# Optimization experiments

Measured on AMD Instinct MI355X. Metric: run time of the kernel, lower is better.

The kernel has to match this reference:

```python
import jax, jax.numpy as jnp
import numpy as np

VOCAB = 50257
D_MEAN = 1024
D_MV = 1024
BATCH = 32
SEQ_LEN = 128


def setup_inputs() -> dict:
    key = jax.random.key(0)
    k_z, k_lab, k_w0, k_w1 = jax.random.split(key, 4)
    z = jax.random.normal(k_z, (BATCH, D_MEAN), dtype=jnp.float32)
    labels = jax.random.randint(k_lab, (BATCH, SEQ_LEN), 0, VOCAB, dtype=jnp.int64)
    # Linear weights stored as [in, out]; scaled like kaiming-uniform-ish init
    W0 = jax.random.normal(k_w0, (D_MEAN, D_MV), dtype=jnp.float32) * (1.0 / np.sqrt(D_MEAN))
    b0 = jnp.zeros((D_MV,), dtype=jnp.float32)
    W1 = jax.random.normal(k_w1, (D_MV, VOCAB), dtype=jnp.float32) * (1.0 / np.sqrt(D_MV))
    b1 = jnp.zeros((VOCAB,), dtype=jnp.float32)
    return {"z": z, "labels": labels, "W0": W0, "b0": b0, "W1": W1, "b1": b1}


def reference(z, labels, W0, b0, W1, b1):
    # bow_head: Linear -> Dropout(eval=identity) -> GELU -> Linear -> Dropout
    h = jax.nn.gelu(z @ W0 + b0, approximate=False)        # [B, d_mean_var]
    logits = h @ W1 + b1                                   # [B, vocab]
    # CrossEntropyLoss over logits expanded across seq_len == mean over
    # (B*seq_len) of NLL; log_softmax computed once per batch row and the
    # label gather reused across seq_len (same math, no expand materialized).
    logp = jax.nn.log_softmax(logits, axis=-1)             # [B, vocab]
    nll = -jnp.take_along_axis(logp, labels, axis=1)       # [B, seq_len]
    return jnp.mean(nll)
```

## Files before the change

kernel.cpp:

```cpp
#include <hip/hip_runtime.h>
#include <math.h>

#define VOCAB 50257
#define DMEAN 1024
#define DMV   1024
#define BATCH 32
#define SEQLEN 128
#define NS1 32
#define NS2 8
#define KC2 (DMV / NS2)
#define CH3 2048
#define VP  51200
#define VPH (VP / 2)
#define NB3 (VP / CH3)

static __device__ inline unsigned f2bf(float x) {
    unsigned u = __float_as_uint(x);
    return (u + 0x7fffu + ((u >> 16) & 1u)) >> 16;
}

__global__ __launch_bounds__(256) void k1_partial(const float* __restrict__ z,
                                                  const float* __restrict__ W0,
                                                  float* __restrict__ part) {
    int tx = threadIdx.x;
    int j  = blockIdx.x * 256 + tx;
    int k0 = blockIdx.y * (DMEAN / NS1);
    float acc[BATCH];
#pragma unroll
    for (int r = 0; r < BATCH; ++r) acc[r] = 0.f;
#pragma unroll 8
    for (int k = k0; k < k0 + (DMEAN / NS1); ++k) {
        float w = W0[k * DMV + j];
#pragma unroll
        for (int r = 0; r < BATCH; ++r)
            acc[r] = fmaf(z[r * DMEAN + k], w, acc[r]);
    }
#pragma unroll
    for (int r = 0; r < BATCH; ++r)
        part[(blockIdx.y * BATCH + r) * DMV + j] = acc[r];
}

__global__ __launch_bounds__(256) void k1_combine(const float* __restrict__ part,
                                                  const float* __restrict__ b0,
                                                  float* __restrict__ hT) {
    int t  = blockIdx.x * 256 + threadIdx.x;
    int e0 = t * 4;
    int r  = e0 >> 10;
    int j  = e0 & 1023;
    float4 s = *(const float4*)(b0 + j);
#pragma unroll
    for (int kb = 0; kb < NS1; ++kb) {
        float4 p = *(const float4*)(part + kb * BATCH * DMV + e0);
        s.x += p.x; s.y += p.y; s.z += p.z; s.w += p.w;
    }
    float v[4] = {s.x, s.y, s.z, s.w};
#pragma unroll
    for (int u = 0; u < 4; ++u) {
        float g = 0.5f * v[u] * (1.f + erff(v[u] * 0.70710678118654752f));
        hT[(j + u) * BATCH + r] = g;
    }
}

__global__ __launch_bounds__(256, 6) void k2_part(const float* __restrict__ hT,
                                                  const float* __restrict__ W1,
                                                  unsigned* __restrict__ part2) {
    __shared__ float hs[KC2 * BATCH];
    int tx = threadIdx.x;
    int n  = blockIdx.x * 256 + tx;
    int nn = min(n, VOCAB - 1);
    int k0 = blockIdx.y * KC2;

    {
        const float4* src = (const float4*)(hT + (size_t)k0 * BATCH);
        float4*       dst = (float4*)hs;
#pragma unroll
        for (int i = 0; i < (KC2 * BATCH / 4) / 256; ++i)
            dst[tx + i * 256] = src[tx + i * 256];
    }
    __syncthreads();

    float acc[BATCH];
#pragma unroll
    for (int r = 0; r < BATCH; ++r) acc[r] = 0.f;

    const float* w = W1 + (size_t)k0 * VOCAB + nn;
#pragma unroll 8
    for (int k = 0; k < KC2; ++k) {
        float wv = w[(size_t)k * VOCAB];
        const float4* hk = (const float4*)(hs + k * BATCH);
        float4 h4[8];
#pragma unroll
        for (int q = 0; q < 8; ++q) h4[q] = hk[q];
        const float* hv = (const float*)h4;
#pragma unroll
        for (int r = 0; r < BATCH; ++r)
            acc[r] = fmaf(hv[r], wv, acc[r]);
    }

    unsigned* p = part2 + (size_t)blockIdx.y * BATCH * VPH + (n >> 1);
    bool even = (tx & 1) == 0;
#pragma unroll
    for (int r = 0; r < BATCH; ++r) {
        float other = __shfl_xor(acc[r], 1, 64);
        unsigned pk = f2bf(acc[r]) | (f2bf(other) << 16);
        if (even) p[(size_t)r * VPH] = pk;
    }
}

__device__ inline float block_reduce_sum(float v, float* red) {
    int tx = threadIdx.x;
#pragma unroll
    for (int off = 32; off > 0; off >>= 1) v += __shfl_down(v, off, 64);
    if ((tx & 63) == 0) red[tx >> 6] = v;
    __syncthreads();
    float res = (red[0] + red[1]) + (red[2] + red[3]);
    __syncthreads();
    return res;
}

__global__ __launch_bounds__(256) void k3_stream(const unsigned* __restrict__ part2,
                                                 const float* __restrict__ b1,
                                                 const int* __restrict__ labels,
                                                 float* __restrict__ se_out,
                                                 float* __restrict__ g_out) {
    __shared__ float sval[CH3];
    __shared__ float red[4];
    int chunk = blockIdx.x, r = blockIdx.y, tx = threadIdx.x;
    int n0 = chunk * CH3 + tx * 8;

    float v[8];
#pragma unroll
    for (int u = 0; u < 8; ++u) v[u] = 0.f;
#pragma unroll
    for (int cs = 0; cs < NS2; ++cs) {
        const unsigned* base = part2 + ((size_t)cs * BATCH + r) * VPH + (n0 >> 1);
        uint4 pv = *(const uint4*)base;
        unsigned pw[4] = {pv.x, pv.y, pv.z, pv.w};
#pragma unroll
        for (int q = 0; q < 4; ++q) {
            v[2 * q]     += __uint_as_float(pw[q] << 16);
            v[2 * q + 1] += __uint_as_float(pw[q] & 0xffff0000u);
        }
    }

    float e = 0.f;
    if (n0 + 7 < VOCAB) {
        float4 ba = *(const float4*)(b1 + n0);
        float4 bb = *(const float4*)(b1 + n0 + 4);
        float bv[8] = {ba.x, ba.y, ba.z, ba.w, bb.x, bb.y, bb.z, bb.w};
#pragma unroll
        for (int u = 0; u < 8; ++u) {
            float lg = v[u] + bv[u];
            sval[tx * 8 + u] = lg;
            e += expf(lg);
        }
    } else {
#pragma unroll
        for (int u = 0; u < 8; ++u) {
            int n = n0 + u;
            float lg = (n < VOCAB) ? (v[u] + b1[n]) : 0.f;
            sval[tx * 8 + u] = lg;
            if (n < VOCAB) e += expf(lg);
        }
    }
    e = block_reduce_sum(e, red);
    if (tx == 0) se_out[r * NB3 + chunk] = e;

    float g = 0.f;
    if (tx < SEQLEN) {
        int lab = labels[r * SEQLEN + tx];
        unsigned d = (unsigned)(lab - chunk * CH3);
        if (d < (unsigned)CH3) g = sval[d];
    }
    g = block_reduce_sum(g, red);
    if (tx == 0) g_out[chunk * BATCH + r] = g;
}

__global__ __launch_bounds__(256) void k4_final(const float* __restrict__ se,
                                                const float* __restrict__ g_part,
                                                float* __restrict__ out) {
    __shared__ float red[4];
    __shared__ float lses[BATCH];
    int tx = threadIdx.x;
    int r = tx >> 3, l8 = tx & 7;
    float s = 0.f;
    for (int c = l8; c < NB3; c += 8) s += se[r * NB3 + c];
#pragma unroll
    for (int off = 4; off > 0; off >>= 1) s += __shfl_down(s, off, 8);
    if (l8 == 0) lses[r] = logf(s);

    float g = 0.f;
    for (int i = tx; i < NB3 * BATCH; i += 256) g += g_part[i];
    g = block_reduce_sum(g, red);

    if (tx == 0) {
        float L = 0.f;
#pragma unroll
        for (int r2 = 0; r2 < BATCH; ++r2) L += lses[r2];
        out[0] = ((float)SEQLEN * L - g) / (float)(BATCH * SEQLEN);
    }
}

extern "C" void kernel_launch(void* const* d_in, const int* in_sizes, int n_in,
                              void* d_out, int out_size, void* d_ws, size_t ws_size,
                              hipStream_t stream) {
    const float* z      = (const float*)d_in[0];
    const int*   labels = (const int*)  d_in[1];
    const float* W0     = (const float*)d_in[2];
    const float* b0     = (const float*)d_in[3];
    const float* W1     = (const float*)d_in[4];
    const float* b1     = (const float*)d_in[5];
    float* out = (float*)d_out;
    float* ws  = (float*)d_ws;

    float*    part1 = ws;
    float*    hT    = part1 + (size_t)NS1 * BATCH * DMV;
    unsigned* part2 = (unsigned*)(hT + (size_t)DMV * BATCH);
    float*    se    = (float*)(part2 + (size_t)NS2 * BATCH * VPH);
    float*    gpart = se + (size_t)BATCH * NB3;

    k1_partial<<<dim3(4, NS1), 256, 0, stream>>>(z, W0, part1);
    k1_combine<<<32, 256, 0, stream>>>(part1, b0, hT);
    k2_part<<<dim3((VOCAB + 255) / 256, NS2), 256, 0, stream>>>(hT, W1, part2);
    k3_stream<<<dim3(NB3, BATCH), 256, 0, stream>>>(part2, b1, labels, se, gpart);
    k4_final<<<1, 256, 0, stream>>>(se, gpart, out);
}
```

Measured before the change: 101.2 us.

## Replace FP32 FMA vocab GEMM with bf16 MFMA using bf16 hidden activations

The second linear layer now runs on the matrix cores via 16x16x32 bf16 MFMA instructions. The hidden activations are stored row-major in bf16, and W1 is loaded as fp32 and converted to bf16 in registers. This targets the scalar-FMA compute bottleneck in the 32x1024x50257 product. It reduces the precision of both operands to bf16, and the strided W1 loads per lane may be less coalesced.

```diff
diff --git a/kernel.cpp b/kernel.cpp
--- a/kernel.cpp
+++ b/kernel.cpp
@@ -14,6 +14,9 @@
 #define VPH (VP / 2)
 #define NB3 (VP / CH3)
 
+typedef __attribute__((ext_vector_type(8))) short short8v;
+typedef __attribute__((ext_vector_type(4))) float f32x4;
+
 static __device__ inline unsigned f2bf(float x) {
     unsigned u = __float_as_uint(x);
     return (u + 0x7fffu + ((u >> 16) & 1u)) >> 16;
@@ -42,7 +45,7 @@
 
 __global__ __launch_bounds__(256) void k1_combine(const float* __restrict__ part,
                                                   const float* __restrict__ b0,
-                                                  float* __restrict__ hT) {
+                                                  unsigned short* __restrict__ hB) {
     int t  = blockIdx.x * 256 + threadIdx.x;
     int e0 = t * 4;
     int r  = e0 >> 10;
@@ -54,56 +57,82 @@
         s.x += p.x; s.y += p.y; s.z += p.z; s.w += p.w;
     }
     float v[4] = {s.x, s.y, s.z, s.w};
+    unsigned b[4];
 #pragma unroll
     for (int u = 0; u < 4; ++u) {
         float g = 0.5f * v[u] * (1.f + erff(v[u] * 0.70710678118654752f));
-        hT[(j + u) * BATCH + r] = g;
-    }
-}
-
-__global__ __launch_bounds__(256, 6) void k2_part(const float* __restrict__ hT,
+        b[u] = f2bf(g);
+    }
+    *(uint2*)(hB + (size_t)r * DMV + j) =
+        make_uint2(b[0] | (b[1] << 16), b[2] | (b[3] << 16));
+}
+
+__global__ __launch_bounds__(256, 4) void k2_mfma(const unsigned short* __restrict__ hB,
                                                   const float* __restrict__ W1,
                                                   unsigned* __restrict__ part2) {
-    __shared__ float hs[KC2 * BATCH];
-    int tx = threadIdx.x;
-    int n  = blockIdx.x * 256 + tx;
-    int nn = min(n, VOCAB - 1);
-    int k0 = blockIdx.y * KC2;
-
-    {
-        const float4* src = (const float4*)(hT + (size_t)k0 * BATCH);
-        float4*       dst = (float4*)hs;
-#pragma unroll
-        for (int i = 0; i < (KC2 * BATCH / 4) / 256; ++i)
-            dst[tx + i * 256] = src[tx + i * 256];
-    }
-    __syncthreads();
-
-    float acc[BATCH];
-#pragma unroll
-    for (int r = 0; r < BATCH; ++r) acc[r] = 0.f;
-
-    const float* w = W1 + (size_t)k0 * VOCAB + nn;
-#pragma unroll 8
-    for (int k = 0; k < KC2; ++k) {
-        float wv = w[(size_t)k * VOCAB];
-        const float4* hk = (const float4*)(hs + k * BATCH);
-        float4 h4[8];
-#pragma unroll
-        for (int q = 0; q < 8; ++q) h4[q] = hk[q];
-        const float* hv = (const float*)h4;
-#pragma unroll
-        for (int r = 0; r < BATCH; ++r)
-            acc[r] = fmaf(hv[r], wv, acc[r]);
-    }
-
-    unsigned* p = part2 + (size_t)blockIdx.y * BATCH * VPH + (n >> 1);
-    bool even = (tx & 1) == 0;
-#pragma unroll
-    for (int r = 0; r < BATCH; ++r) {
-        float other = __shfl_xor(acc[r], 1, 64);
-        unsigned pk = f2bf(acc[r]) | (f2bf(other) << 16);
-        if (even) p[(size_t)r * VPH] = pk;
+    int tx   = threadIdx.x;
+    int lane = tx & 63;
+    int w    = tx >> 6;
+    int lr   = lane & 15;
+    int lg   = lane >> 4;
+    int k0   = blockIdx.y * KC2;
+    int col0 = blockIdx.x * 256 + w * 64;
+
+    short8v a[2][4];
+#pragma unroll
+    for (int m = 0; m < 2; ++m)
+#pragma unroll
+        for (int t = 0; t < 4; ++t) {
+            const unsigned* hp =
+                (const unsigned*)(hB + (size_t)(m * 16 + lr) * DMV + k0 + t * 32 + lg * 4);
+            union { short8v v; unsigned u[4]; } A;
+            A.u[0] = hp[0];  A.u[1] = hp[1];
+            A.u[2] = hp[8];  A.u[3] = hp[9];
+            a[m][t] = A.v;
+        }
+
+    f32x4 acc[4][2];
+#pragma unroll
+    for (int c = 0; c < 4; ++c)
+#pragma unroll
+        for (int m = 0; m < 2; ++m)
+            acc[c][m] = (f32x4){0.f, 0.f, 0.f, 0.f};
+
+#pragma unroll
+    for (int c = 0; c < 4; ++c) {
+        unsigned colc = (unsigned)min(col0 + c * 16 + lr, VOCAB - 1);
+        const float* wl = W1 + (size_t)(k0 + lg * 4) * VOCAB + colc;
+#pragma unroll
+        for (int t = 0; t < 4; ++t) {
+            float fv[8];
+#pragma unroll
+            for (int r = 0; r < 8; ++r)
+                fv[r] = wl[(size_t)(t * 32 + (r & 3) + 16 * (r >> 2)) * VOCAB];
+            union { short8v v; unsigned u[4]; } B;
+#pragma unroll
+            for (int q = 0; q < 4; ++q)
+                B.u[q] = f2bf(fv[2 * q]) | (f2bf(fv[2 * q + 1]) << 16);
+            acc[c][0] = __builtin_amdgcn_mfma_f32_16x16x32_bf16(a[0][t], B.v, acc[c][0], 0, 0, 0);
+            acc[c][1] = __builtin_amdgcn_mfma_f32_16x16x32_bf16(a[1][t], B.v, acc[c][1], 0, 0, 0);
+        }
+    }
+
+    unsigned* pb = part2 + (size_t)blockIdx.y * BATCH * VPH;
+#pragma unroll
+    for (int c = 0; c < 4; ++c) {
+        int col = col0 + c * 16 + lr;
+#pragma unroll
+        for (int m = 0; m < 2; ++m) {
+            int row0 = m * 16 + lg * 4;
+#pragma unroll
+            for (int j = 0; j < 4; ++j) {
+                float v = acc[c][m][j];
+                float o = __shfl_xor(v, 1, 64);
+                if (!(lane & 1))
+                    pb[(size_t)(row0 + j) * VPH + (col >> 1)] =
+                        f2bf(v) | (f2bf(o) << 16);
+            }
+        }
     }
 }
 
@@ -213,15 +242,15 @@
     float* out = (float*)d_out;
     float* ws  = (float*)d_ws;
 
-    float*    part1 = ws;
-    float*    hT    = part1 + (size_t)NS1 * BATCH * DMV;
-    unsigned* part2 = (unsigned*)(hT + (size_t)DMV * BATCH);
-    float*    se    = (float*)(part2 + (size_t)NS2 * BATCH * VPH);
-    float*    gpart = se + (size_t)BATCH * NB3;
+    float*          part1 = ws;
+    unsigned short* hB    = (unsigned short*)(part1 + (size_t)NS1 * BATCH * DMV);
+    unsigned*       part2 = (unsigned*)(hB + (size_t)BATCH * DMV);
+    float*          se    = (float*)(part2 + (size_t)NS2 * BATCH * VPH);
+    float*          gpart = se + (size_t)BATCH * NB3;
 
     k1_partial<<<dim3(4, NS1), 256, 0, stream>>>(z, W0, part1);
-    k1_combine<<<32, 256, 0, stream>>>(part1, b0, hT);
-    k2_part<<<dim3((VOCAB + 255) / 256, NS2), 256, 0, stream>>>(hT, W1, part2);
+    k1_combine<<<32, 256, 0, stream>>>(part1, b0, hB);
+    k2_mfma<<<dim3((VOCAB + 255) / 256, NS2), 256, 0, stream>>>(hB, W1, part2);
     k3_stream<<<dim3(NB3, BATCH), 256, 0, stream>>>(part2, b1, labels, se, gpart);
     k4_final<<<1, 256, 0, stream>>>(se, gpart, out);
 }
```

Result: slower. 122.1 us (+20.6%).
